# Kernel optimization log

Hardware: AMD Instinct MI355X
Metric: run time of the kernel (lower is better)

## Reference

```python
import jax, jax.numpy as jnp
import numpy as np

IN_MODES = (4, 4, 8, 8, 4)
OUT_MODES = (4, 4, 8, 8, 4)
RANKS = (1, 8, 8, 8, 8, 1)
N_TOKENS = 8192


def setup_inputs() -> dict:
    key = jax.random.key(0)
    ks = jax.random.split(key, 7)
    inp = jax.random.normal(ks[0], (N_TOKENS, int(np.prod(IN_MODES))), dtype=jnp.float32)
    cores = []
    for i in range(5):
        shape = (IN_MODES[i], RANKS[i], RANKS[i + 1], OUT_MODES[i])
        # kaiming-uniform-like small init to keep the 5-core chain numerically tame
        fan_in = shape[0] * shape[1] * shape[2]
        bound = float(np.sqrt(3.0 / fan_in))
        cores.append(jax.random.uniform(ks[i + 1], shape, minval=-bound, maxval=bound, dtype=jnp.float32))
    biases = jax.random.uniform(ks[6], (int(np.prod(OUT_MODES)),), minval=-0.05, maxval=0.05, dtype=jnp.float32)
    return {
        "input": inp,
        "core0": cores[0], "core1": cores[1], "core2": cores[2],
        "core3": cores[3], "core4": cores[4],
        "biases": biases,
    }


def reference(input, core0, core1, core2, core3, core4, biases):
    # reshape tokens into the 5 input modes: [N, a, b, c, d, e]
    x = input.reshape((-1,) + IN_MODES)
    # TT contraction. Original einsum has no '->'; free indices h (ranks[0]=1)
    # and m (ranks[5]=1) are size-1 boundary ranks, so summing them out here is
    # equivalent to the original reshape-squeeze.
    out = jnp.einsum(
        'nabcde,ahiv,bijw,cjkx,dkly,elmz->nvwxyz',
        x, core0, core1, core2, core3, core4,
        optimize='optimal',
    )
    out = out.reshape(-1, int(np.prod(OUT_MODES)))
    return out + biases
```

## Files before the change

kernel.cpp:

```cpp
#include <hip/hip_runtime.h>

#define DIM 4096

typedef __bf16 bf16x8 __attribute__((ext_vector_type(8)));
typedef float floatx4 __attribute__((ext_vector_type(4)));


__global__ void build_small(const float* __restrict__ c0, const float* __restrict__ c1,
                            const float* __restrict__ c3, const float* __restrict__ c4,
                            float* __restrict__ K01, float* __restrict__ K34T) {
  int t = blockIdx.x * 256 + threadIdx.x;
  if (t < 2048) {
    int vw = t & 15, j = (t >> 4) & 7, ab = t >> 7;
    int a = ab >> 2, b = ab & 3, v = vw >> 2, w = vw & 3;
    float s = 0.f;
#pragma unroll
    for (int i = 0; i < 8; ++i)
      s += c0[a * 32 + i * 4 + v] * c1[b * 256 + i * 32 + j * 4 + w];
    K01[t] = s;
  } else if (t < 2048 + 8192) {
    int u = t - 2048;
    int yz = u & 31, k = (u >> 5) & 7, de = u >> 8;
    int d = de >> 2, e = de & 3, y = yz >> 2, z = yz & 3;
    float s = 0.f;
#pragma unroll
    for (int l = 0; l < 8; ++l)
      s += c3[d * 512 + k * 64 + l * 8 + y] * c4[e * 32 + l * 4 + z];
    K34T[k * 1024 + yz * 32 + de] = s;
  }
}

__global__ void build_k012(const float* __restrict__ K01, const float* __restrict__ c2,
                           float* __restrict__ K012) {
  int t = blockIdx.x * 256 + threadIdx.x;
  int vwx = t & 127, k = (t >> 7) & 7, abc = t >> 10;
  int ab = abc >> 3, c = abc & 7, vw = vwx >> 3, x = vwx & 7;
  float s = 0.f;
#pragma unroll
  for (int j = 0; j < 8; ++j)
    s += K01[ab * 128 + j * 16 + vw] * c2[c * 512 + j * 64 + k * 8 + x];
  K012[t] = s;
}

__global__ void build_wt(const float* __restrict__ K012, const float* __restrict__ K34T,
                         __bf16* __restrict__ WT) {
  int t = blockIdx.x * 256 + threadIdx.x;
  int in = t & 4095, o = t >> 12;
  int de = in & 31, abc = in >> 5;
  int yz = o & 31, vwx = o >> 5;
  float s = 0.f;
#pragma unroll
  for (int k = 0; k < 8; ++k)
    s += K012[abc * 1024 + k * 128 + vwx] * K34T[k * 1024 + yz * 32 + de];
  WT[t] = (__bf16)s;
}

__global__ void x_to_bf16(const float* __restrict__ X, __bf16* __restrict__ Xb) {
  long t = (long)blockIdx.x * 256 + threadIdx.x;
  float4 a = ((const float4*)X)[t * 2];
  float4 b = ((const float4*)X)[t * 2 + 1];
  bf16x8 w;
  w[0] = (__bf16)a.x; w[1] = (__bf16)a.y; w[2] = (__bf16)a.z; w[3] = (__bf16)a.w;
  w[4] = (__bf16)b.x; w[5] = (__bf16)b.y; w[6] = (__bf16)b.z; w[7] = (__bf16)b.w;
  ((bf16x8*)Xb)[t] = w;
}

__device__ __forceinline__ void async_ld16(void* lds, const void* g) {
  __builtin_amdgcn_global_load_lds(
      (const __attribute__((address_space(1))) unsigned int*)g,
      (__attribute__((address_space(3))) unsigned int*)lds, 16, 0, 0);
}

__global__ __launch_bounds__(256) void gemm_bf(const __bf16* __restrict__ A,
                                               const __bf16* __restrict__ WT,
                                               const float* __restrict__ bias,
                                               float* __restrict__ C) {
  __shared__ __bf16 As[128 * 64];
  __shared__ __bf16 Bs[128 * 64];

  const int tid = threadIdx.x;
  const int n0 = (blockIdx.x & 31) * 128;
  const int m0 = (blockIdx.x >> 5) * 128;

  const int wave = tid >> 6, lane = tid & 63;
  const int wm = (wave >> 1) * 64, wn = (wave & 1) * 64;
  const int lm = lane & 15, kq = lane >> 4;

  floatx4 acc[4][4] = {};

  const __bf16* agp[4];
  const __bf16* bgp[4];
  int ldsoff[4];
#pragma unroll
  for (int j = 0; j < 4; ++j) {
    int q = tid + j * 256;
    int r = q >> 3, pc = q & 7;
    int c = pc ^ (r & 7);
    ldsoff[j] = q * 8;
    agp[j] = A + (long)(m0 + r) * DIM + c * 8;
    bgp[j] = WT + (long)(n0 + r) * DIM + c * 8;
  }

#pragma unroll 1
  for (int k0 = 0; k0 < DIM; k0 += 64) {
#pragma unroll
    for (int j = 0; j < 4; ++j) async_ld16(&As[ldsoff[j]], agp[j] + k0);
#pragma unroll
    for (int j = 0; j < 4; ++j) async_ld16(&Bs[ldsoff[j]], bgp[j] + k0);
    __syncthreads();

#pragma unroll
    for (int kh = 0; kh < 2; ++kh) {
      bf16x8 af[4], bfr[4];
#pragma unroll
      for (int mi = 0; mi < 4; ++mi) {
        int r = wm + mi * 16 + lm;
        int pc = (kh * 4 + kq) ^ (r & 7);
        af[mi] = *(const bf16x8*)&As[r * 64 + pc * 8];
      }
#pragma unroll
      for (int ni = 0; ni < 4; ++ni) {
        int r = wn + ni * 16 + lm;
        int pc = (kh * 4 + kq) ^ (r & 7);
        bfr[ni] = *(const bf16x8*)&Bs[r * 64 + pc * 8];
      }
#pragma unroll
      for (int mi = 0; mi < 4; ++mi)
#pragma unroll
        for (int ni = 0; ni < 4; ++ni)
          acc[mi][ni] = __builtin_amdgcn_mfma_f32_16x16x32_bf16(af[mi], bfr[ni], acc[mi][ni], 0, 0, 0);
    }
    __syncthreads();
  }

  float bv[4];
#pragma unroll
  for (int ni = 0; ni < 4; ++ni) bv[ni] = bias[n0 + wn + ni * 16 + lm];
#pragma unroll
  for (int mi = 0; mi < 4; ++mi) {
    long mr = m0 + wm + mi * 16 + kq * 4;
#pragma unroll
    for (int ni = 0; ni < 4; ++ni) {
      float* cp = C + mr * DIM + (n0 + wn + ni * 16 + lm);
      cp[0]       = acc[mi][ni][0] + bv[ni];
      cp[DIM]     = acc[mi][ni][1] + bv[ni];
      cp[2 * DIM] = acc[mi][ni][2] + bv[ni];
      cp[3 * DIM] = acc[mi][ni][3] + bv[ni];
    }
  }
}

__global__ __launch_bounds__(256) void gemm_xw(const float* __restrict__ X,
                                               const __bf16* __restrict__ WT,
                                               const float* __restrict__ bias,
                                               float* __restrict__ C) {
  __shared__ __bf16 As[128 * 40];
  __shared__ __bf16 Bs[128 * 32];

  const int tid = threadIdx.x;
  const int n0 = (blockIdx.x & 31) * 128;
  const int m0 = (blockIdx.x >> 5) * 128;

  const int wave = tid >> 6, lane = tid & 63;
  const int wm = (wave >> 1) * 64, wn = (wave & 1) * 64;
  const int lm = lane & 15, kq = lane >> 4;

  floatx4 acc[4][4] = {};

  const int ar = tid >> 1;
  const int ac = (tid & 1) * 16;
  const float* xp = X + (long)(m0 + ar) * DIM + ac;
  __bf16* as_dst = &As[ar * 40 + ac];

  const int u0 = tid, u1 = 256 + tid;
  const int r0 = u0 >> 2, r1 = u1 >> 2;
  const int ch0 = (u0 & 3) ^ (r0 & 3), ch1 = (u1 & 3) ^ (r1 & 3);
  const __bf16* wp0 = WT + (long)(n0 + r0) * DIM + ch0 * 8;
  const __bf16* wp1 = WT + (long)(n0 + r1) * DIM + ch1 * 8;

  float4 a0 = *(const float4*)(xp);
  float4 a1 = *(const float4*)(xp + 4);
  float4 a2 = *(const float4*)(xp + 8);
  float4 a3 = *(const float4*)(xp + 12);

#pragma unroll 1
  for (int k0 = 0; k0 < DIM; k0 += 32) {
    async_ld16(&Bs[u0 * 8], wp0 + k0);
    async_ld16(&Bs[u1 * 8], wp1 + k0);

    bf16x8 w0, w1;
    w0[0] = (__bf16)a0.x; w0[1] = (__bf16)a0.y; w0[2] = (__bf16)a0.z; w0[3] = (__bf16)a0.w;
    w0[4] = (__bf16)a1.x; w0[5] = (__bf16)a1.y; w0[6] = (__bf16)a1.z; w0[7] = (__bf16)a1.w;
    w1[0] = (__bf16)a2.x; w1[1] = (__bf16)a2.y; w1[2] = (__bf16)a2.z; w1[3] = (__bf16)a2.w;
    w1[4] = (__bf16)a3.x; w1[5] = (__bf16)a3.y; w1[6] = (__bf16)a3.z; w1[7] = (__bf16)a3.w;
    *(bf16x8*)(as_dst) = w0;
    *(bf16x8*)(as_dst + 8) = w1;

    if (k0 + 32 < DIM) {
      a0 = *(const float4*)(xp + k0 + 32);
      a1 = *(const float4*)(xp + k0 + 36);
      a2 = *(const float4*)(xp + k0 + 40);
      a3 = *(const float4*)(xp + k0 + 44);
    }
    __syncthreads();

    bf16x8 af[4], bfr[4];
#pragma unroll
    for (int mi = 0; mi < 4; ++mi)
      af[mi] = *(const bf16x8*)&As[(wm + mi * 16 + lm) * 40 + kq * 8];
#pragma unroll
    for (int ni = 0; ni < 4; ++ni) {
      int rr = wn + ni * 16 + lm;
      bfr[ni] = *(const bf16x8*)&Bs[rr * 32 + ((kq ^ (rr & 3)) * 8)];
    }
#pragma unroll
    for (int mi = 0; mi < 4; ++mi)
#pragma unroll
      for (int ni = 0; ni < 4; ++ni)
        acc[mi][ni] = __builtin_amdgcn_mfma_f32_16x16x32_bf16(af[mi], bfr[ni], acc[mi][ni], 0, 0, 0);
    __syncthreads();
  }

  float bv[4];
#pragma unroll
  for (int ni = 0; ni < 4; ++ni) bv[ni] = bias[n0 + wn + ni * 16 + lm];
#pragma unroll
  for (int mi = 0; mi < 4; ++mi) {
    long mr = m0 + wm + mi * 16 + kq * 4;
#pragma unroll
    for (int ni = 0; ni < 4; ++ni) {
      float* cp = C + mr * DIM + (n0 + wn + ni * 16 + lm);
      cp[0]       = acc[mi][ni][0] + bv[ni];
      cp[DIM]     = acc[mi][ni][1] + bv[ni];
      cp[2 * DIM] = acc[mi][ni][2] + bv[ni];
      cp[3 * DIM] = acc[mi][ni][3] + bv[ni];
    }
  }
}

extern "C" void kernel_launch(void* const* d_in, const int* in_sizes, int n_in,
                              void* d_out, int out_size, void* d_ws, size_t ws_size,
                              hipStream_t stream) {
  const float* x    = (const float*)d_in[0];
  const float* c0   = (const float*)d_in[1];
  const float* c1   = (const float*)d_in[2];
  const float* c2   = (const float*)d_in[3];
  const float* c3   = (const float*)d_in[4];
  const float* c4   = (const float*)d_in[5];
  const float* bias = (const float*)d_in[6];
  float* out = (float*)d_out;

  const size_t XB_SZ = 67108864;
  const size_t WT_SZ = 33554432;
  const size_t K012_SZ = 524288;
  const size_t K01_SZ = 8192;
  const size_t K34_SZ = 32768;
  char* ws = (char*)d_ws;

  if (ws_size >= XB_SZ + WT_SZ + K012_SZ + K01_SZ + K34_SZ) {
    __bf16* Xb  = (__bf16*)ws;
    __bf16* WT  = (__bf16*)(ws + XB_SZ);
    float* K012 = (float*)(ws + XB_SZ + WT_SZ);
    float* K01  = (float*)(ws + XB_SZ + WT_SZ + K012_SZ);
    float* K34T = (float*)(ws + XB_SZ + WT_SZ + K012_SZ + K01_SZ);

    build_small<<<40, 256, 0, stream>>>(c0, c1, c3, c4, K01, K34T);
    x_to_bf16<<<16384, 256, 0, stream>>>(x, Xb);
    build_k012<<<512, 256, 0, stream>>>(K01, c2, K012);
    build_wt<<<65536, 256, 0, stream>>>(K012, K34T, WT);
    gemm_bf<<<2048, 256, 0, stream>>>(Xb, WT, bias, out);
  } else {
    __bf16* WT  = (__bf16*)ws;
    float* K012 = (float*)(ws + WT_SZ);
    float* K01  = (float*)(ws + WT_SZ + K012_SZ);
    float* K34T = (float*)(ws + WT_SZ + K012_SZ + K01_SZ);

    build_small<<<40, 256, 0, stream>>>(c0, c1, c3, c4, K01, K34T);
    build_k012<<<512, 256, 0, stream>>>(K01, c2, K012);
    build_wt<<<65536, 256, 0, stream>>>(K012, K34T, WT);
    gemm_xw<<<2048, 256, 0, stream>>>(x, WT, bias, out);
  }
}
```

Measured before the change: 554.4 us.

## Fuse weight-build kernels and replace GEMM with 256x256 eight-phase pipelined kernel

```diff
diff --git a/kernel.cpp b/kernel.cpp
--- a/kernel.cpp
+++ b/kernel.cpp
@@ -4,66 +4,6 @@
 
 typedef __bf16 bf16x8 __attribute__((ext_vector_type(8)));
 typedef float floatx4 __attribute__((ext_vector_type(4)));
-
-
-__global__ void build_small(const float* __restrict__ c0, const float* __restrict__ c1,
-                            const float* __restrict__ c3, const float* __restrict__ c4,
-                            float* __restrict__ K01, float* __restrict__ K34T) {
-  int t = blockIdx.x * 256 + threadIdx.x;
-  if (t < 2048) {
-    int vw = t & 15, j = (t >> 4) & 7, ab = t >> 7;
-    int a = ab >> 2, b = ab & 3, v = vw >> 2, w = vw & 3;
-    float s = 0.f;
-#pragma unroll
-    for (int i = 0; i < 8; ++i)
-      s += c0[a * 32 + i * 4 + v] * c1[b * 256 + i * 32 + j * 4 + w];
-    K01[t] = s;
-  } else if (t < 2048 + 8192) {
-    int u = t - 2048;
-    int yz = u & 31, k = (u >> 5) & 7, de = u >> 8;
-    int d = de >> 2, e = de & 3, y = yz >> 2, z = yz & 3;
-    float s = 0.f;
-#pragma unroll
-    for (int l = 0; l < 8; ++l)
-      s += c3[d * 512 + k * 64 + l * 8 + y] * c4[e * 32 + l * 4 + z];
-    K34T[k * 1024 + yz * 32 + de] = s;
-  }
-}
-
-__global__ void build_k012(const float* __restrict__ K01, const float* __restrict__ c2,
-                           float* __restrict__ K012) {
-  int t = blockIdx.x * 256 + threadIdx.x;
-  int vwx = t & 127, k = (t >> 7) & 7, abc = t >> 10;
-  int ab = abc >> 3, c = abc & 7, vw = vwx >> 3, x = vwx & 7;
-  float s = 0.f;
-#pragma unroll
-  for (int j = 0; j < 8; ++j)
-    s += K01[ab * 128 + j * 16 + vw] * c2[c * 512 + j * 64 + k * 8 + x];
-  K012[t] = s;
-}
-
-__global__ void build_wt(const float* __restrict__ K012, const float* __restrict__ K34T,
-                         __bf16* __restrict__ WT) {
-  int t = blockIdx.x * 256 + threadIdx.x;
-  int in = t & 4095, o = t >> 12;
-  int de = in & 31, abc = in >> 5;
-  int yz = o & 31, vwx = o >> 5;
-  float s = 0.f;
-#pragma unroll
-  for (int k = 0; k < 8; ++k)
-    s += K012[abc * 1024 + k * 128 + vwx] * K34T[k * 1024 + yz * 32 + de];
-  WT[t] = (__bf16)s;
-}
-
-__global__ void x_to_bf16(const float* __restrict__ X, __bf16* __restrict__ Xb) {
-  long t = (long)blockIdx.x * 256 + threadIdx.x;
-  float4 a = ((const float4*)X)[t * 2];
-  float4 b = ((const float4*)X)[t * 2 + 1];
-  bf16x8 w;
-  w[0] = (__bf16)a.x; w[1] = (__bf16)a.y; w[2] = (__bf16)a.z; w[3] = (__bf16)a.w;
-  w[4] = (__bf16)b.x; w[5] = (__bf16)b.y; w[6] = (__bf16)b.z; w[7] = (__bf16)b.w;
-  ((bf16x8*)Xb)[t] = w;
-}
 
 __device__ __forceinline__ void async_ld16(void* lds, const void* g) {
   __builtin_amdgcn_global_load_lds(
@@ -71,81 +11,212 @@
       (__attribute__((address_space(3))) unsigned int*)lds, 16, 0, 0);
 }
 
-__global__ __launch_bounds__(256) void gemm_bf(const __bf16* __restrict__ A,
-                                               const __bf16* __restrict__ WT,
-                                               const float* __restrict__ bias,
-                                               float* __restrict__ C) {
-  __shared__ __bf16 As[128 * 64];
-  __shared__ __bf16 Bs[128 * 64];
+__global__ void build_k(const float* __restrict__ c0, const float* __restrict__ c1,
+                        const float* __restrict__ c2, const float* __restrict__ c3,
+                        const float* __restrict__ c4,
+                        float* __restrict__ K012, float* __restrict__ K34T) {
+  const int bid = blockIdx.x, tid = threadIdx.x;
+  if (bid < 512) {
+    __shared__ float K01s[128];
+    const int abc = bid >> 2;
+    const int ab = abc >> 3, c = abc & 7;
+    if (tid < 128) {
+      const int a = ab >> 2, b = ab & 3;
+      const int j = tid >> 4, vw = tid & 15, v = vw >> 2, w = vw & 3;
+      float s = 0.f;
+#pragma unroll
+      for (int i = 0; i < 8; ++i)
+        s += c0[a * 32 + i * 4 + v] * c1[b * 256 + i * 32 + j * 4 + w];
+      K01s[tid] = s;
+    }
+    __syncthreads();
+    const int t = bid * 256 + tid;
+    const int vwx = t & 127, k = (t >> 7) & 7;
+    const int vw = vwx >> 3, xx = vwx & 7;
+    float s = 0.f;
+#pragma unroll
+    for (int j = 0; j < 8; ++j)
+      s += K01s[j * 16 + vw] * c2[c * 512 + j * 64 + k * 8 + xx];
+    K012[t] = s;
+  } else {
+    const int u = (bid - 512) * 256 + tid;
+    const int yz = u & 31, kk = (u >> 5) & 7, de = u >> 8;
+    const int d = de >> 2, e = de & 3, y = yz >> 2, z = yz & 3;
+    float s = 0.f;
+#pragma unroll
+    for (int l = 0; l < 8; ++l)
+      s += c3[d * 512 + kk * 64 + l * 8 + y] * c4[e * 32 + l * 4 + z];
+    K34T[kk * 1024 + yz * 32 + de] = s;
+  }
+}
+
+__global__ void build_wt_conv(const float* __restrict__ K012, const float* __restrict__ K34T,
+                              __bf16* __restrict__ WT,
+                              const float* __restrict__ X, __bf16* __restrict__ Xb) {
+  const int bid = blockIdx.x, tid = threadIdx.x;
+  if (bid < 8192) {
+    const long t = (long)bid * 256 + tid;
+    const long e8 = t * 8;
+    const int in = (int)(e8 & 4095), o = (int)(e8 >> 12);
+    const int de0 = in & 31, abc = in >> 5;
+    const int yz = o & 31, vwx = o >> 5;
+    const float* kp = K012 + abc * 1024 + vwx;
+    const float* vp = K34T + yz * 32 + de0;
+    float s[8] = {};
+#pragma unroll
+    for (int k = 0; k < 8; ++k) {
+      const float a = kp[k * 128];
+      const float4 v0 = *(const float4*)(vp + k * 1024);
+      const float4 v1 = *(const float4*)(vp + k * 1024 + 4);
+      s[0] += a * v0.x; s[1] += a * v0.y; s[2] += a * v0.z; s[3] += a * v0.w;
+      s[4] += a * v1.x; s[5] += a * v1.y; s[6] += a * v1.z; s[7] += a * v1.w;
+    }
+    bf16x8 w;
+#pragma unroll
+    for (int d = 0; d < 8; ++d) w[d] = (__bf16)s[d];
+    ((bf16x8*)WT)[t] = w;
+  } else {
+    const long t = (long)(bid - 8192) * 256 + tid;
+    const float4 a = ((const float4*)X)[t * 2];
+    const float4 b = ((const float4*)X)[t * 2 + 1];
+    bf16x8 w;
+    w[0] = (__bf16)a.x; w[1] = (__bf16)a.y; w[2] = (__bf16)a.z; w[3] = (__bf16)a.w;
+    w[4] = (__bf16)b.x; w[5] = (__bf16)b.y; w[6] = (__bf16)b.z; w[7] = (__bf16)b.w;
+    ((bf16x8*)Xb)[t] = w;
+  }
+}
+
+
+#define G_BAR1() do { __builtin_amdgcn_s_barrier(); \
+                      asm volatile("s_waitcnt lgkmcnt(0)" ::: "memory"); \
+                      __builtin_amdgcn_sched_barrier(0); } while (0)
+#define G_BAR2() do { __builtin_amdgcn_s_barrier(); \
+                      __builtin_amdgcn_sched_barrier(0); } while (0)
+#define G_VM6()  asm volatile("s_waitcnt vmcnt(6)" ::: "memory")
+
+#define G_STA(p, h, koff) do { \
+  async_ld16(&As[p][(h) * 128][0] + ldsq[0], agp[0] + (h) * 524288 + (koff)); \
+  async_ld16(&As[p][(h) * 128][0] + ldsq[1], agp[1] + (h) * 524288 + (koff)); } while (0)
+#define G_STB(p, h, koff) do { \
+  async_ld16(&Bs[p][(h) * 128][0] + ldsq[0], bgp[0] + (h) * 524288 + (koff)); \
+  async_ld16(&Bs[p][(h) * 128][0] + ldsq[1], bgp[1] + (h) * 524288 + (koff)); } while (0)
+
+#define G_LDA(p, mh) do { \
+  _Pragma("unroll") for (int fi = 0; fi < 4; ++fi) { \
+    const int row = ((mh) * 8 + 2 * fi + wm) * 16 + lm; \
+    _Pragma("unroll") for (int kh = 0; kh < 2; ++kh) \
+      af[fi][kh] = *(const bf16x8*)&As[p][row][((kh * 4 + kq) ^ (row & 7)) * 8]; \
+  } } while (0)
+#define G_LDB(p, nh) do { \
+  _Pragma("unroll") for (int gi = 0; gi < 2; ++gi) { \
+    const int g = (nh) * 2 + gi; \
+    const int row = (4 * g + wn) * 16 + lm; \
+    _Pragma("unroll") for (int kh = 0; kh < 2; ++kh) \
+      bfv[g][kh] = *(const bf16x8*)&Bs[p][row][((kh * 4 + kq) ^ (row & 7)) * 8]; \
+  } } while (0)
+
+#define G_MMA(mh, nh) do { \
+  __builtin_amdgcn_s_setprio(1); \
+  _Pragma("unroll") for (int fi = 0; fi < 4; ++fi) \
+  _Pragma("unroll") for (int gi = 0; gi < 2; ++gi) \
+  _Pragma("unroll") for (int kh = 0; kh < 2; ++kh) \
+    acc[(mh) * 4 + fi][(nh) * 2 + gi] = __builtin_amdgcn_mfma_f32_16x16x32_bf16( \
+        af[fi][kh], bfv[(nh) * 2 + gi][kh], acc[(mh) * 4 + fi][(nh) * 2 + gi], 0, 0, 0); \
+  __builtin_amdgcn_s_setprio(0); } while (0)
+
+__global__ __launch_bounds__(512, 2) void gemm_8ph(const __bf16* __restrict__ A,
+                                                   const __bf16* __restrict__ WT,
+                                                   const float* __restrict__ bias,
+                                                   float* __restrict__ C) {
+  __shared__ __bf16 As[2][256][64];
+  __shared__ __bf16 Bs[2][256][64];
 
   const int tid = threadIdx.x;
-  const int n0 = (blockIdx.x & 31) * 128;
-  const int m0 = (blockIdx.x >> 5) * 128;
+  const int gb = (blockIdx.x & 7) * 64 + (blockIdx.x >> 3);
+  const int m0 = (gb >> 4) * 256;
+  const int n0 = (gb & 15) * 256;
 
   const int wave = tid >> 6, lane = tid & 63;
-  const int wm = (wave >> 1) * 64, wn = (wave & 1) * 64;
+  const int wm = wave & 1, wn = wave >> 1;
   const int lm = lane & 15, kq = lane >> 4;
 
-  floatx4 acc[4][4] = {};
-
-  const __bf16* agp[4];
-  const __bf16* bgp[4];
-  int ldsoff[4];
-#pragma unroll
-  for (int j = 0; j < 4; ++j) {
-    int q = tid + j * 256;
-    int r = q >> 3, pc = q & 7;
-    int c = pc ^ (r & 7);
-    ldsoff[j] = q * 8;
+  floatx4 acc[8][4] = {};
+  bf16x8 af[4][2], bfv[4][2];
+
+  const __bf16* agp[2];
+  const __bf16* bgp[2];
+  int ldsq[2];
+#pragma unroll
+  for (int j = 0; j < 2; ++j) {
+    const int q = tid + j * 512;
+    const int r = q >> 3, pc = q & 7;
+    const int c = pc ^ (r & 7);
+    ldsq[j] = q * 8;
     agp[j] = A + (long)(m0 + r) * DIM + c * 8;
     bgp[j] = WT + (long)(n0 + r) * DIM + c * 8;
   }
 
+  G_STA(0, 0, 0); G_STB(0, 0, 0); G_STB(0, 1, 0); G_STA(0, 1, 0);
+  G_STA(1, 0, 64); G_STB(1, 0, 64); G_STB(1, 1, 64);
+  G_VM6();
+  __builtin_amdgcn_s_barrier();
+  __builtin_amdgcn_sched_barrier(0);
+
 #pragma unroll 1
-  for (int k0 = 0; k0 < DIM; k0 += 64) {
-#pragma unroll
-    for (int j = 0; j < 4; ++j) async_ld16(&As[ldsoff[j]], agp[j] + k0);
-#pragma unroll
-    for (int j = 0; j < 4; ++j) async_ld16(&Bs[ldsoff[j]], bgp[j] + k0);
-    __syncthreads();
-
-#pragma unroll
-    for (int kh = 0; kh < 2; ++kh) {
-      bf16x8 af[4], bfr[4];
-#pragma unroll
-      for (int mi = 0; mi < 4; ++mi) {
-        int r = wm + mi * 16 + lm;
-        int pc = (kh * 4 + kq) ^ (r & 7);
-        af[mi] = *(const bf16x8*)&As[r * 64 + pc * 8];
-      }
-#pragma unroll
-      for (int ni = 0; ni < 4; ++ni) {
-        int r = wn + ni * 16 + lm;
-        int pc = (kh * 4 + kq) ^ (r & 7);
-        bfr[ni] = *(const bf16x8*)&Bs[r * 64 + pc * 8];
-      }
-#pragma unroll
-      for (int mi = 0; mi < 4; ++mi)
-#pragma unroll
-        for (int ni = 0; ni < 4; ++ni)
-          acc[mi][ni] = __builtin_amdgcn_mfma_f32_16x16x32_bf16(af[mi], bfr[ni], acc[mi][ni], 0, 0, 0);
-    }
-    __syncthreads();
+  for (int it = 0; it < 32; ++it) {
+    const int kA = (2 * it + 1) * 64;
+    int t2 = 2 * it + 2; if (t2 > 63) t2 = 63;
+    int t3 = 2 * it + 3; if (t3 > 63) t3 = 63;
+    const int kB = t2 * 64, kC = t3 * 64;
+
+    G_LDA(0, 0); G_LDB(0, 0);
+    G_STA(1, 1, kA);
+    G_BAR1(); G_MMA(0, 0); G_BAR2();
+
+    G_LDB(0, 1);
+    G_STA(0, 0, kB);
+    G_BAR1(); G_MMA(0, 1); G_BAR2();
+
+    G_LDA(0, 1);
+    G_STB(0, 0, kB);
+    G_BAR1(); G_MMA(1, 0); G_BAR2();
+
+    G_STB(0, 1, kB);
+    G_BAR1(); G_MMA(1, 1);
+    G_VM6();
+    G_BAR2();
+
+    G_LDA(1, 0); G_LDB(1, 0);
+    G_STA(0, 1, kB);
+    G_BAR1(); G_MMA(0, 0); G_BAR2();
+
+    G_LDB(1, 1);
+    G_STA(1, 0, kC);
+    G_BAR1(); G_MMA(0, 1); G_BAR2();
+
+    G_LDA(1, 1);
+    G_STB(1, 0, kC);
+    G_BAR1(); G_MMA(1, 0); G_BAR2();
+
+    G_STB(1, 1, kC);
+    G_BAR1(); G_MMA(1, 1);
+    G_VM6();
+    G_BAR2();
   }
 
   float bv[4];
 #pragma unroll
-  for (int ni = 0; ni < 4; ++ni) bv[ni] = bias[n0 + wn + ni * 16 + lm];
-#pragma unroll
-  for (int mi = 0; mi < 4; ++mi) {
-    long mr = m0 + wm + mi * 16 + kq * 4;
-#pragma unroll
-    for (int ni = 0; ni < 4; ++ni) {
-      float* cp = C + mr * DIM + (n0 + wn + ni * 16 + lm);
-      cp[0]       = acc[mi][ni][0] + bv[ni];
-      cp[DIM]     = acc[mi][ni][1] + bv[ni];
-      cp[2 * DIM] = acc[mi][ni][2] + bv[ni];
-      cp[3 * DIM] = acc[mi][ni][3] + bv[ni];
+  for (int g = 0; g < 4; ++g) bv[g] = bias[n0 + (4 * g + wn) * 16 + lm];
+#pragma unroll
+  for (int f = 0; f < 8; ++f) {
+    const long mr = m0 + (2 * f + wm) * 16 + kq * 4;
+#pragma unroll
+    for (int g = 0; g < 4; ++g) {
+      float* cp = C + mr * DIM + n0 + (4 * g + wn) * 16 + lm;
+      cp[0]       = acc[f][g][0] + bv[g];
+      cp[DIM]     = acc[f][g][1] + bv[g];
+      cp[2 * DIM] = acc[f][g][2] + bv[g];
+      cp[3 * DIM] = acc[f][g][3] + bv[g];
     }
   }
 }
@@ -154,8 +225,8 @@
                                                const __bf16* __restrict__ WT,
                                                const float* __restrict__ bias,
                                                float* __restrict__ C) {
-  __shared__ __bf16 As[128 * 40];
-  __shared__ __bf16 Bs[128 * 32];
+  __shared__ __bf16 Asf[128 * 40];
+  __shared__ __bf16 Bsf[128 * 32];
 
   const int tid = threadIdx.x;
   const int n0 = (blockIdx.x & 31) * 128;
@@ -170,7 +241,7 @@
   const int ar = tid >> 1;
   const int ac = (tid & 1) * 16;
   const float* xp = X + (long)(m0 + ar) * DIM + ac;
-  __bf16* as_dst = &As[ar * 40 + ac];
+  __bf16* as_dst = &Asf[ar * 40 + ac];
 
   const int u0 = tid, u1 = 256 + tid;
   const int r0 = u0 >> 2, r1 = u1 >> 2;
@@ -185,8 +256,8 @@
 
 #pragma unroll 1
   for (int k0 = 0; k0 < DIM; k0 += 32) {
-    async_ld16(&Bs[u0 * 8], wp0 + k0);
-    async_ld16(&Bs[u1 * 8], wp1 + k0);
+    async_ld16(&Bsf[u0 * 8], wp0 + k0);
+    async_ld16(&Bsf[u1 * 8], wp1 + k0);
 
     bf16x8 w0, w1;
     w0[0] = (__bf16)a0.x; w0[1] = (__bf16)a0.y; w0[2] = (__bf16)a0.z; w0[3] = (__bf16)a0.w;
@@ -204,20 +275,20 @@
     }
     __syncthreads();
 
-    bf16x8 af[4], bfr[4];
+    bf16x8 afv[4], bfr[4];
 #pragma unroll
     for (int mi = 0; mi < 4; ++mi)
-      af[mi] = *(const bf16x8*)&As[(wm + mi * 16 + lm) * 40 + kq * 8];
+      afv[mi] = *(const bf16x8*)&Asf[(wm + mi * 16 + lm) * 40 + kq * 8];
 #pragma unroll
     for (int ni = 0; ni < 4; ++ni) {
       int rr = wn + ni * 16 + lm;
-      bfr[ni] = *(const bf16x8*)&Bs[rr * 32 + ((kq ^ (rr & 3)) * 8)];
+      bfr[ni] = *(const bf16x8*)&Bsf[rr * 32 + ((kq ^ (rr & 3)) * 8)];
     }
 #pragma unroll
     for (int mi = 0; mi < 4; ++mi)
 #pragma unroll
       for (int ni = 0; ni < 4; ++ni)
-        acc[mi][ni] = __builtin_amdgcn_mfma_f32_16x16x32_bf16(af[mi], bfr[ni], acc[mi][ni], 0, 0, 0);
+        acc[mi][ni] = __builtin_amdgcn_mfma_f32_16x16x32_bf16(afv[mi], bfr[ni], acc[mi][ni], 0, 0, 0);
     __syncthreads();
   }
 
@@ -253,31 +324,25 @@
   const size_t XB_SZ = 67108864;
   const size_t WT_SZ = 33554432;
   const size_t K012_SZ = 524288;
-  const size_t K01_SZ = 8192;
   const size_t K34_SZ = 32768;
   char* ws = (char*)d_ws;
 
-  if (ws_size >= XB_SZ + WT_SZ + K012_SZ + K01_SZ + K34_SZ) {
+  if (ws_size >= XB_SZ + WT_SZ + K012_SZ + K34_SZ) {
     __bf16* Xb  = (__bf16*)ws;
     __bf16* WT  = (__bf16*)(ws + XB_SZ);
     float* K012 = (float*)(ws + XB_SZ + WT_SZ);
-    float* K01  = (float*)(ws + XB_SZ + WT_SZ + K012_SZ);
-    float* K34T = (float*)(ws + XB_SZ + WT_SZ + K012_SZ + K01_SZ);
-
-    build_small<<<40, 256, 0, stream>>>(c0, c1, c3, c4, K01, K34T);
-    x_to_bf16<<<16384, 256, 0, stream>>>(x, Xb);
-    build_k012<<<512, 256, 0, stream>>>(K01, c2, K012);
-    build_wt<<<65536, 256, 0, stream>>>(K012, K34T, WT);
-    gemm_bf<<<2048, 256, 0, stream>>>(Xb, WT, bias, out);
+    float* K34T = (float*)(ws + XB_SZ + WT_SZ + K012_SZ);
+
+    build_k<<<544, 256, 0, stream>>>(c0, c1, c2, c3, c4, K012, K34T);
+    build_wt_conv<<<24576, 256, 0, stream>>>(K012, K34T, WT, x, Xb);
+    gemm_8ph<<<512, 512, 0, stream>>>(Xb, WT, bias, out);
   } else {
     __bf16* WT  = (__bf16*)ws;
     float* K012 = (float*)(ws + WT_SZ);
-    float* K01  = (float*)(ws + WT_SZ + K012_SZ);
-    float* K34T = (float*)(ws + WT_SZ + K012_SZ + K01_SZ);
-
-    build_small<<<40, 256, 0, stream>>>(c0, c1, c3, c4, K01, K34T);
-    build_k012<<<512, 256, 0, stream>>>(K01, c2, K012);
-    build_wt<<<65536, 256, 0, stream>>>(K012, K34T, WT);
+    float* K34T = (float*)(ws + WT_SZ + K012_SZ);
+
+    build_k<<<544, 256, 0, stream>>>(c0, c1, c2, c3, c4, K012, K34T);
+    build_wt_conv<<<8192, 256, 0, stream>>>(K012, K34T, WT, x, (__bf16*)nullptr);
     gemm_xw<<<2048, 256, 0, stream>>>(x, WT, bias, out);
   }
 }
```

Result: faster. 486.7 us (-12.2%).
